# Kernel tuning notes

Hardware: AMD Instinct MI355X
Metric: run time of the kernel (lower is better)

## Reference

```python
import jax, jax.numpy as jnp
import numpy as np

N_NODES = 100_000
N_EDGES = 1_600_000
F_NODE = 16
F_EDGE = 8
HID = 128
N_GRAPHS = 2048


def setup_inputs() -> dict:
    key = jax.random.key(0)
    ks = jax.random.split(key, 20)
    inp = {
        "node_attr": jax.random.normal(ks[0], (N_NODES, F_NODE), dtype=jnp.float32),
        "edge_attr": jax.random.normal(ks[1], (N_EDGES, F_EDGE), dtype=jnp.float32),
        "edge_index": jax.random.randint(ks[2], (2, N_EDGES), 0, N_NODES),
        "adj_index": jax.random.randint(ks[3], (2, N_EDGES), 0, N_NODES),
        "adj_value": jax.random.uniform(ks[4], (N_EDGES,), dtype=jnp.float32) * 0.1,
        "batch": jnp.sort(jax.random.randint(ks[5], (N_NODES,), 0, N_GRAPHS)),
    }
    def glorot(k, shape):
        fan_in, fan_out = shape[0], shape[1]
        std = jnp.sqrt(2.0 / (fan_in + fan_out)).astype(jnp.float32)
        return jax.random.normal(k, shape, dtype=jnp.float32) * std
    # attr embedder params
    inp["W_node"] = glorot(ks[6], (F_NODE, HID))
    inp["W_edge"] = glorot(ks[7], (F_EDGE, HID))
    inp["b_embed"] = jnp.zeros((HID,), dtype=jnp.float32)
    # 3 GCN layers
    inp["W1"] = glorot(ks[8], (HID, HID)); inp["b1"] = jnp.zeros((HID,), jnp.float32)
    inp["W2"] = glorot(ks[9], (HID, HID)); inp["b2"] = jnp.zeros((HID,), jnp.float32)
    inp["W3"] = glorot(ks[10], (HID, HID)); inp["b3"] = jnp.zeros((HID,), jnp.float32)
    # predictor MLP
    inp["Wp1"] = glorot(ks[11], (HID, HID)); inp["bp1"] = jnp.full((HID,), 0.01, jnp.float32)
    inp["Wp2"] = glorot(ks[12], (HID, 1));   inp["bp2"] = jnp.full((1,), 0.01, jnp.float32)
    return inp


def _forward(node_attr, edge_attr, adj_value,
             W_node, W_edge, b_embed, W1, b1, W2, b2, W3, b3,
             Wp1, bp1, Wp2, bp2, edge_index, adj_index, batch):
    # --- attr embedder: mix node feats with edge feats scattered to dst nodes ---
    he = edge_attr @ W_edge                                   # [E, H]
    agg = jax.ops.segment_sum(he, edge_index[1], num_segments=N_NODES)
    h = jax.nn.relu(node_attr @ W_node + agg + b_embed)       # [N, H]

    # --- GCN stack: h <- relu(tilde_A @ (h W) + b) via sparse COO SpMM ---
    src, dst = adj_index[0], adj_index[1]
    def gcn(h, W, b):
        hw = h @ W + b                                        # [N, H]
        msg = adj_value[:, None] * hw[dst]                    # [E, H] gather
        return jax.nn.relu(jax.ops.segment_sum(msg, src, num_segments=N_NODES))
    h = gcn(h, W1, b1)
    h = gcn(h, W2, b2)
    h = gcn(h, W3, b3)

    # --- global_add_pool over graphs ---
    fp = jax.ops.segment_sum(h, batch, num_segments=N_GRAPHS)  # [G, H]

    # --- predictor MLP ---
    z = jax.nn.relu(fp @ Wp1 + bp1)
    return z @ Wp2 + bp2                                       # [G, 1]


def reference(node_attr, edge_attr, edge_index, adj_index, adj_value, batch,
              W_node, W_edge, b_embed, W1, b1, W2, b2, W3, b3,
              Wp1, bp1, Wp2, bp2):
    return _forward(node_attr, edge_attr, adj_value,
                    W_node, W_edge, b_embed, W1, b1, W2, b2, W3, b3,
                    Wp1, bp1, Wp2, bp2, edge_index, adj_index, batch)
```

## Files before the change

### kernel.cpp

```cpp
#include <hip/hip_runtime.h>

#define H 128
#define FN 16
#define FE 8
#define NBUK_MAX 1600

__global__ __launch_bounds__(256) void k_hist2_gb(
    const int* __restrict__ k1, const int* __restrict__ k2,
    int* __restrict__ bcnt1, int* __restrict__ bcnt2, int E, int nbuk,
    const int* __restrict__ batch, int* __restrict__ gstart, int N, int G) {
  if (blockIdx.x >= 512) {
    int n = (blockIdx.x - 512) * 256 + threadIdx.x;
    if (n > N) return;
    if (n == 0) {
      for (int g = 0; g <= batch[0]; g++) gstart[g] = 0;
    } else if (n == N) {
      for (int g = batch[N - 1] + 1; g <= G; g++) gstart[g] = N;
    } else {
      int b0 = batch[n - 1], b1 = batch[n];
      for (int g = b0 + 1; g <= b1; g++) gstart[g] = n;
    }
    return;
  }
  __shared__ int h1[NBUK_MAX], h2[NBUK_MAX];
  for (int i = threadIdx.x; i < nbuk; i += 256) { h1[i] = 0; h2[i] = 0; }
  __syncthreads();
  for (int e = blockIdx.x * 256 + threadIdx.x; e < E; e += 512 * 256) {
    atomicAdd(&h1[k1[e] >> 6], 1);
    atomicAdd(&h2[k2[e] >> 6], 1);
  }
  __syncthreads();
  for (int i = threadIdx.x; i < nbuk; i += 256) {
    if (h1[i]) atomicAdd(&bcnt1[i], h1[i]);
    if (h2[i]) atomicAdd(&bcnt2[i], h2[i]);
  }
}

__global__ __launch_bounds__(1024) void k_scan(
    const int* __restrict__ cnt1, int* __restrict__ st1, int* __restrict__ gc1,
    const int* __restrict__ cnt2, int* __restrict__ st2, int* __restrict__ gc2,
    int nbuk) {
  __shared__ int s[1024];
  int tid = threadIdx.x;
  for (int pass = 0; pass < 2; pass++) {
    const int* cnt = pass ? cnt2 : cnt1;
    int* st = pass ? st2 : st1;
    int* gc = pass ? gc2 : gc1;
    int run = 0;
    for (int half = 0; half * 1024 < nbuk; half++) {
      int i = half * 1024 + tid;
      int v = (i < nbuk) ? cnt[i] : 0;
      s[tid] = v; __syncthreads();
      for (int off = 1; off < 1024; off <<= 1) {
        int t = (tid >= off) ? s[tid - off] : 0;
        __syncthreads();
        s[tid] += t;
        __syncthreads();
      }
      int excl = run + s[tid] - v;
      if (i < nbuk) { st[i] = excl; gc[i] = excl; }
      run += s[1023];
      __syncthreads();
    }
    if (tid == 0) st[nbuk] = run;
    __syncthreads();
  }
}

__global__ __launch_bounds__(256) void k_p1_both(
    const int* __restrict__ k1, const int* __restrict__ adj, const float* __restrict__ vals,
    int* __restrict__ gcur1, int* __restrict__ gcur2,
    int* __restrict__ pkey, int2* __restrict__ bpay, int E, int nbuk, int p1b) {
  __shared__ int hc[NBUK_MAX];
  int tid = threadIdx.x;
  bool packed = (int)blockIdx.x < p1b;
  int chunk = packed ? blockIdx.x : blockIdx.x - p1b;
  const int* key = packed ? k1 : adj;
  int* gcur = packed ? gcur1 : gcur2;
  int c0 = chunk * 8192;
  int c1 = min(c0 + 8192, E);
  for (int i = tid; i < nbuk; i += 256) hc[i] = 0;
  __syncthreads();
  for (int e = c0 + tid; e < c1; e += 256)
    atomicAdd(&hc[key[e] >> 6], 1);
  __syncthreads();
  for (int i = tid; i < nbuk; i += 256) {
    int c = hc[i];
    if (c) hc[i] = atomicAdd(&gcur[i], c);
  }
  __syncthreads();
  if (packed) {
    for (int e = c0 + tid; e < c1; e += 256) {
      int k = key[e];
      int pos = atomicAdd(&hc[k >> 6], 1);
      pkey[pos] = (e << 6) | (k & 63);
    }
  } else {
    const int* dsts = adj + E;
    for (int e = c0 + tid; e < c1; e += 256) {
      int k = key[e];
      int pos = atomicAdd(&hc[k >> 6], 1);
      bpay[pos] = make_int2(dsts[e] | ((k & 63) << 20), __float_as_int(vals[e]));
    }
  }
}

__global__ __launch_bounds__(256) void k_agg_p2(
    const int* __restrict__ pkey, const float* __restrict__ edge_attr,
    const int* __restrict__ bst1,
    const float* __restrict__ node_attr, const float* __restrict__ Wn,
    const float* __restrict__ We8, const float* __restrict__ bemb,
    float* __restrict__ hout,
    const int2* __restrict__ bpay, const int* __restrict__ bst2,
    int* __restrict__ offs, int2* __restrict__ payF, float* __restrict__ rs,
    int N, int E, int nbuk) {
  __shared__ float lds[FE][64];
  __shared__ float na[64][FN];
  __shared__ int cnt[64], scn[64], cur[64];
  __shared__ float vsum[64];
  int tid = threadIdx.x;

  if ((int)blockIdx.x < nbuk) {
    int b = blockIdx.x;
    int node0 = b * 64;
    int col = tid & 127;
    int half = tid >> 7;
    float wreg[FN + FE];
#pragma unroll
    for (int k = 0; k < FN; k++) wreg[k] = Wn[k * H + col];
#pragma unroll
    for (int k = 0; k < FE; k++) wreg[FN + k] = We8[k * H + col];
    float bcol = bemb[col];

    for (int i = tid; i < FE * 64; i += 256) ((float*)lds)[i] = 0.f;
    for (int i = tid; i < 64 * FN; i += 256) {
      int n = node0 + (i >> 4);
      na[i >> 4][i & 15] = (n < N) ? node_attr[(size_t)n * FN + (i & 15)] : 0.f;
    }
    __syncthreads();
    int s = bst1[b], t = bst1[b + 1];
    int i = s + tid;
    for (; i + 256 < t; i += 512) {
      int pk0 = pkey[i], pk1 = pkey[i + 256];
      const float4* e0 = (const float4*)(edge_attr + (size_t)(pk0 >> 6) * FE);
      const float4* e1 = (const float4*)(edge_attr + (size_t)(pk1 >> 6) * FE);
      float4 a0 = e0[0], b0 = e0[1], a1 = e1[0], b1 = e1[1];
      int s0 = pk0 & 63, s1 = pk1 & 63;
      atomicAdd(&lds[0][s0], a0.x);  atomicAdd(&lds[1][s0], a0.y);
      atomicAdd(&lds[2][s0], a0.z);  atomicAdd(&lds[3][s0], a0.w);
      atomicAdd(&lds[4][s0], b0.x);  atomicAdd(&lds[5][s0], b0.y);
      atomicAdd(&lds[6][s0], b0.z);  atomicAdd(&lds[7][s0], b0.w);
      atomicAdd(&lds[0][s1], a1.x);  atomicAdd(&lds[1][s1], a1.y);
      atomicAdd(&lds[2][s1], a1.z);  atomicAdd(&lds[3][s1], a1.w);
      atomicAdd(&lds[4][s1], b1.x);  atomicAdd(&lds[5][s1], b1.y);
      atomicAdd(&lds[6][s1], b1.z);  atomicAdd(&lds[7][s1], b1.w);
    }
    for (; i < t; i += 256) {
      int pk = pkey[i];
      int e = pk >> 6, slot = pk & 63;
      const float4* ea = (const float4*)(edge_attr + (size_t)e * FE);
      float4 a = ea[0], b4 = ea[1];
      atomicAdd(&lds[0][slot], a.x);  atomicAdd(&lds[1][slot], a.y);
      atomicAdd(&lds[2][slot], a.z);  atomicAdd(&lds[3][slot], a.w);
      atomicAdd(&lds[4][slot], b4.x); atomicAdd(&lds[5][slot], b4.y);
      atomicAdd(&lds[6][slot], b4.z); atomicAdd(&lds[7][slot], b4.w);
    }
    __syncthreads();
    for (int pr = 0; pr < 32; pr++) {
      int nl = pr * 2 + half;
      int n = node0 + nl;
      float acc = bcol;
#pragma unroll
      for (int k = 0; k < FN; k++) acc += na[nl][k] * wreg[k];
#pragma unroll
      for (int k = 0; k < FE; k++) acc += lds[k][nl] * wreg[FN + k];
      if (n < N) hout[(size_t)n * H + col] = fmaxf(acc, 0.f);
    }
  } else {
    int b = blockIdx.x - nbuk;
    int s = bst2[b], t = bst2[b + 1];
    if (tid < 64) { cnt[tid] = 0; vsum[tid] = 0.f; }
    __syncthreads();
    for (int i = s + tid; i < t; i += 256) atomicAdd(&cnt[(bpay[i].x >> 20) & 63], 1);
    __syncthreads();
    if (tid < 64) scn[tid] = cnt[tid];
    __syncthreads();
    for (int off = 1; off < 64; off <<= 1) {
      int v = 0;
      if (tid < 64 && tid >= off) v = scn[tid - off];
      __syncthreads();
      if (tid < 64 && tid >= off) scn[tid] += v;
      __syncthreads();
    }
    if (tid < 64) {
      int excl = s + scn[tid] - cnt[tid];
      cur[tid] = excl;
      int node = b * 64 + tid;
      if (node < N) offs[node] = excl;
    }
    if (b == 0 && tid == 0) offs[N] = E;
    __syncthreads();
    for (int i = s + tid; i < t; i += 256) {
      int2 p = bpay[i];
      int slot = (p.x >> 20) & 63;
      int pos = atomicAdd(&cur[slot], 1);
      payF[pos] = make_int2(p.x & 0xFFFFF, p.y);
      atomicAdd(&vsum[slot], __int_as_float(p.y));
    }
    __syncthreads();
    if (tid < 64) {
      int node = b * 64 + tid;
      if (node < N) rs[node] = vsum[tid];
    }
  }
}

__global__ __launch_bounds__(256) void k_fused(
    const float* __restrict__ h, const int* __restrict__ offs,
    const int2* __restrict__ pay, const float* __restrict__ W,
    const float* __restrict__ bias, const float* __restrict__ rs,
    float* __restrict__ out, int N) {
  __shared__ float4 hs4[32 * 32];
  int tid = threadIdx.x;
  int c  = tid & 31;
  int rg = tid >> 5;
  int base = blockIdx.x * 32;
  const float4* h4 = (const float4*)h;

  for (int r = 0; r < 4; r++) {
    int row = rg * 4 + r;
    int n = base + row;
    float4 a0 = make_float4(0.f, 0.f, 0.f, 0.f);
    float4 a1 = make_float4(0.f, 0.f, 0.f, 0.f);
    float4 a2 = make_float4(0.f, 0.f, 0.f, 0.f);
    float4 a3 = make_float4(0.f, 0.f, 0.f, 0.f);
    if (n < N) {
      int s = offs[n], t = offs[n + 1];
      int i = s, t4 = s + ((t - s) & ~3);
      for (; i < t4; i += 4) {
        int2 p0 = pay[i], p1 = pay[i + 1], p2 = pay[i + 2], p3 = pay[i + 3];
        float4 h0 = h4[(size_t)p0.x * 32 + c];
        float4 h1 = h4[(size_t)p1.x * 32 + c];
        float4 h2 = h4[(size_t)p2.x * 32 + c];
        float4 h3 = h4[(size_t)p3.x * 32 + c];
        float v0 = __int_as_float(p0.y), v1 = __int_as_float(p1.y);
        float v2 = __int_as_float(p2.y), v3 = __int_as_float(p3.y);
        a0.x += v0 * h0.x; a0.y += v0 * h0.y; a0.z += v0 * h0.z; a0.w += v0 * h0.w;
        a1.x += v1 * h1.x; a1.y += v1 * h1.y; a1.z += v1 * h1.z; a1.w += v1 * h1.w;
        a2.x += v2 * h2.x; a2.y += v2 * h2.y; a2.z += v2 * h2.z; a2.w += v2 * h2.w;
        a3.x += v3 * h3.x; a3.y += v3 * h3.y; a3.z += v3 * h3.z; a3.w += v3 * h3.w;
      }
      for (; i < t; i++) {
        int2 p = pay[i];
        float v = __int_as_float(p.y);
        float4 hv = h4[(size_t)p.x * 32 + c];
        a0.x += v * hv.x; a0.y += v * hv.y; a0.z += v * hv.z; a0.w += v * hv.w;
      }
    }
    hs4[row * 32 + c] = make_float4(a0.x + a1.x + a2.x + a3.x,
                                    a0.y + a1.y + a2.y + a3.y,
                                    a0.z + a1.z + a2.z + a3.z,
                                    a0.w + a1.w + a2.w + a3.w);
  }
  __syncthreads();

  const float4* W4 = (const float4*)W;
  float4 acc[4];
#pragma unroll
  for (int i = 0; i < 4; i++) acc[i] = make_float4(0.f, 0.f, 0.f, 0.f);
#pragma unroll 2
  for (int k = 0; k < 32; k++) {
    float4 w0 = W4[(k * 4 + 0) * 32 + c];
    float4 w1 = W4[(k * 4 + 1) * 32 + c];
    float4 w2 = W4[(k * 4 + 2) * 32 + c];
    float4 w3 = W4[(k * 4 + 3) * 32 + c];
#pragma unroll
    for (int i = 0; i < 4; i++) {
      float4 hv = hs4[(rg + 8 * i) * 32 + k];
      acc[i].x += hv.x * w0.x + hv.y * w1.x + hv.z * w2.x + hv.w * w3.x;
      acc[i].y += hv.x * w0.y + hv.y * w1.y + hv.z * w2.y + hv.w * w3.y;
      acc[i].z += hv.x * w0.z + hv.y * w1.z + hv.z * w2.z + hv.w * w3.z;
      acc[i].w += hv.x * w0.w + hv.y * w1.w + hv.z * w2.w + hv.w * w3.w;
    }
  }

  float4 bv = ((const float4*)bias)[c];
#pragma unroll
  for (int i = 0; i < 4; i++) {
    int row = rg + 8 * i;
    int n = base + row;
    if (n < N) {
      float rsv = rs[n];
      float4 o;
      o.x = fmaxf(acc[i].x + rsv * bv.x, 0.f);
      o.y = fmaxf(acc[i].y + rsv * bv.y, 0.f);
      o.z = fmaxf(acc[i].z + rsv * bv.z, 0.f);
      o.w = fmaxf(acc[i].w + rsv * bv.w, 0.f);
      ((float4*)out)[(size_t)n * 32 + c] = o;
    }
  }
}

__global__ __launch_bounds__(256) void k_gemm_pred(
    const float* __restrict__ in, const float* __restrict__ W,
    const float* __restrict__ bias, const float* __restrict__ Wp2,
    const float* __restrict__ bp2, float* __restrict__ out, int N) {
  __shared__ float4 hs4[64 * 32];
  int tid = threadIdx.x;
  int c  = tid & 31;
  int rg = tid >> 5;
  int rowBase = blockIdx.x * 64;
  const float4* in4 = (const float4*)in;
  const float4* W4  = (const float4*)W;
#pragma unroll
  for (int j = 0; j < 8; j++) {
    int q = tid + 256 * j;
    int r = rowBase + (q >> 5);
    int rr = (r < N) ? r : (N - 1);
    hs4[q] = in4[(size_t)rr * 32 + (q & 31)];
  }
  __syncthreads();
  float4 acc[8];
#pragma unroll
  for (int i = 0; i < 8; i++) acc[i] = make_float4(0.f, 0.f, 0.f, 0.f);
#pragma unroll 2
  for (int k = 0; k < 32; k++) {
    float4 w0 = W4[(k * 4 + 0) * 32 + c];
    float4 w1 = W4[(k * 4 + 1) * 32 + c];
    float4 w2 = W4[(k * 4 + 2) * 32 + c];
    float4 w3 = W4[(k * 4 + 3) * 32 + c];
#pragma unroll
    for (int i = 0; i < 8; i++) {
      float4 hv = hs4[(rg + 8 * i) * 32 + k];
      acc[i].x += hv.x * w0.x + hv.y * w1.x + hv.z * w2.x + hv.w * w3.x;
      acc[i].y += hv.x * w0.y + hv.y * w1.y + hv.z * w2.y + hv.w * w3.y;
      acc[i].z += hv.x * w0.z + hv.y * w1.z + hv.z * w2.z + hv.w * w3.z;
      acc[i].w += hv.x * w0.w + hv.y * w1.w + hv.z * w2.w + hv.w * w3.w;
    }
  }
  float4 bv = ((const float4*)bias)[c];
  float4 wp = ((const float4*)Wp2)[c];
  float bp = bp2[0];
#pragma unroll
  for (int i = 0; i < 8; i++) {
    int row = rowBase + rg + 8 * i;
    float4 o;
    o.x = fmaxf(acc[i].x + bv.x, 0.f);
    o.y = fmaxf(acc[i].y + bv.y, 0.f);
    o.z = fmaxf(acc[i].z + bv.z, 0.f);
    o.w = fmaxf(acc[i].w + bv.w, 0.f);
    float v = o.x * wp.x + o.y * wp.y + o.z * wp.z + o.w * wp.w;
#pragma unroll
    for (int off = 16; off > 0; off >>= 1) v += __shfl_down(v, off, 32);
    if (c == 0 && row < N) out[row] = v + bp;
  }
}

__global__ __launch_bounds__(256) void k_pool_seg(
    const float* __restrict__ h, const int* __restrict__ gstart,
    float* __restrict__ fp, int G) {
  __shared__ float4 red[8][32];
  int g = blockIdx.x;
  int c = threadIdx.x & 31, rg = threadIdx.x >> 5;
  int s = gstart[g], t = gstart[g + 1];
  const float4* h4 = (const float4*)h;
  float4 a = make_float4(0.f, 0.f, 0.f, 0.f);
  for (int n = s + rg; n < t; n += 8) {
    float4 v = h4[(size_t)n * 32 + c];
    a.x += v.x; a.y += v.y; a.z += v.z; a.w += v.w;
  }
  red[rg][c] = a;
  __syncthreads();
  if (rg == 0) {
    float4 r = red[0][c];
#pragma unroll
    for (int j = 1; j < 8; j++) {
      float4 v = red[j][c];
      r.x += v.x; r.y += v.y; r.z += v.z; r.w += v.w;
    }
    ((float4*)fp)[(size_t)g * 32 + c] = r;
  }
}

extern "C" void kernel_launch(void* const* d_in, const int* in_sizes, int n_in,
                              void* d_out, int out_size, void* d_ws, size_t ws_size,
                              hipStream_t stream) {
  const float* node_attr  = (const float*)d_in[0];
  const float* edge_attr  = (const float*)d_in[1];
  const int*   edge_index = (const int*)d_in[2];
  const int*   adj_index  = (const int*)d_in[3];
  const float* adj_value  = (const float*)d_in[4];
  const int*   batch      = (const int*)d_in[5];
  const float* W_node  = (const float*)d_in[6];
  const float* W_edge  = (const float*)d_in[7];
  const float* b_embed = (const float*)d_in[8];
  const float* W1 = (const float*)d_in[9];
  const float* b1 = (const float*)d_in[10];
  const float* W2 = (const float*)d_in[11];
  const float* b2 = (const float*)d_in[12];
  const float* W3 = (const float*)d_in[13];
  const float* b3 = (const float*)d_in[14];
  const float* Wp1 = (const float*)d_in[15];
  const float* bp1 = (const float*)d_in[16];
  const float* Wp2 = (const float*)d_in[17];
  const float* bp2 = (const float*)d_in[18];
  float* out = (float*)d_out;

  const int E = in_sizes[4];
  const int N = in_sizes[5];
  const int G = out_size;
  const int nbuk = (N + 63) >> 6;
  const int p1b = (E + 8191) / 8192;
  const int gbB = (N + 256) / 256;

  float* A     = (float*)d_ws;
  float* B     = A + (size_t)N * H;
  int2*  payF  = (int2*)(B + (size_t)N * H);
  float* fpool = (float*)(payF + E);
  int*   bcnt1 = (int*)(fpool + (size_t)G * H);
  int*   bcnt2 = bcnt1 + nbuk;
  int*   bst1  = bcnt2 + nbuk;
  int*   gcur1 = bst1 + nbuk + 1;
  int*   bst2  = gcur1 + nbuk;
  int*   gcur2 = bst2 + nbuk + 1;
  int*   offs2 = gcur2 + nbuk;
  int*   gstart= offs2 + N + 1;
  float* rs    = (float*)(gstart + G + 1);
  int*   pkey  = (int*)B;
  int2*  bpay2 = (int2*)(((int*)B) + E);

  hipMemsetAsync(bcnt1, 0, (size_t)2 * nbuk * sizeof(int), stream);
  k_hist2_gb<<<512 + gbB, 256, 0, stream>>>(edge_index + E, adj_index, bcnt1, bcnt2,
                                            E, nbuk, batch, gstart, N, G);
  k_scan<<<1, 1024, 0, stream>>>(bcnt1, bst1, gcur1, bcnt2, bst2, gcur2, nbuk);

  k_p1_both<<<2 * p1b, 256, 0, stream>>>(edge_index + E, adj_index, adj_value,
                                         gcur1, gcur2, pkey, bpay2, E, nbuk, p1b);

  k_agg_p2<<<2 * nbuk, 256, 0, stream>>>(pkey, edge_attr, bst1,
                                         node_attr, W_node, W_edge, b_embed, A,
                                         bpay2, bst2, offs2, payF, rs, N, E, nbuk);

  int lb = (N + 31) / 32;
  k_fused<<<lb, 256, 0, stream>>>(A, offs2, payF, W1, b1, rs, B, N);
  k_fused<<<lb, 256, 0, stream>>>(B, offs2, payF, W2, b2, rs, A, N);
  k_fused<<<lb, 256, 0, stream>>>(A, offs2, payF, W3, b3, rs, B, N);

  k_pool_seg<<<G, 256, 0, stream>>>(B, gstart, fpool, G);
  k_gemm_pred<<<(G + 63) / 64, 256, 0, stream>>>(fpool, Wp1, bp1, Wp2, bp2, out, G);
}
```

Baseline: 900.7 us.

## Fuse global add pool into final GCN layer and enlarge node tile to 64

The last GCN layer now pools its outputs directly: each block reduces its 64 rows per graph in shared memory and atomically adds the result into the pooled buffer, so the final layer output never goes to global memory and the separate pool kernel and gstart computation are dropped. The fused SpMM+GEMM kernels also process 64 nodes per block instead of 32, which reuses each W load across more rows but doubles accumulator registers and shared memory per block. The pooled buffer is now zeroed by the existing memset, and float atomics make the pooled sums order-nondeterministic.

After: 856.3 us. 4.9% less time.

```diff
diff --git a/kernel.cpp b/kernel.cpp
--- a/kernel.cpp
+++ b/kernel.cpp
@@ -5,23 +5,9 @@
 #define FE 8
 #define NBUK_MAX 1600
 
-__global__ __launch_bounds__(256) void k_hist2_gb(
+__global__ __launch_bounds__(256) void k_hist2(
     const int* __restrict__ k1, const int* __restrict__ k2,
-    int* __restrict__ bcnt1, int* __restrict__ bcnt2, int E, int nbuk,
-    const int* __restrict__ batch, int* __restrict__ gstart, int N, int G) {
-  if (blockIdx.x >= 512) {
-    int n = (blockIdx.x - 512) * 256 + threadIdx.x;
-    if (n > N) return;
-    if (n == 0) {
-      for (int g = 0; g <= batch[0]; g++) gstart[g] = 0;
-    } else if (n == N) {
-      for (int g = batch[N - 1] + 1; g <= G; g++) gstart[g] = N;
-    } else {
-      int b0 = batch[n - 1], b1 = batch[n];
-      for (int g = b0 + 1; g <= b1; g++) gstart[g] = n;
-    }
-    return;
-  }
+    int* __restrict__ bcnt1, int* __restrict__ bcnt2, int E, int nbuk) {
   __shared__ int h1[NBUK_MAX], h2[NBUK_MAX];
   for (int i = threadIdx.x; i < nbuk; i += 256) { h1[i] = 0; h2[i] = 0; }
   __syncthreads();
@@ -220,15 +206,15 @@
     const int2* __restrict__ pay, const float* __restrict__ W,
     const float* __restrict__ bias, const float* __restrict__ rs,
     float* __restrict__ out, int N) {
-  __shared__ float4 hs4[32 * 32];
+  __shared__ float4 hs4[64 * 32];
   int tid = threadIdx.x;
   int c  = tid & 31;
   int rg = tid >> 5;
-  int base = blockIdx.x * 32;
+  int base = blockIdx.x * 64;
   const float4* h4 = (const float4*)h;
 
-  for (int r = 0; r < 4; r++) {
-    int row = rg * 4 + r;
+  for (int r = 0; r < 8; r++) {
+    int row = rg * 8 + r;
     int n = base + row;
     float4 a0 = make_float4(0.f, 0.f, 0.f, 0.f);
     float4 a1 = make_float4(0.f, 0.f, 0.f, 0.f);
@@ -265,9 +251,9 @@
   __syncthreads();
 
   const float4* W4 = (const float4*)W;
-  float4 acc[4];
-#pragma unroll
-  for (int i = 0; i < 4; i++) acc[i] = make_float4(0.f, 0.f, 0.f, 0.f);
+  float4 acc[8];
+#pragma unroll
+  for (int i = 0; i < 8; i++) acc[i] = make_float4(0.f, 0.f, 0.f, 0.f);
 #pragma unroll 2
   for (int k = 0; k < 32; k++) {
     float4 w0 = W4[(k * 4 + 0) * 32 + c];
@@ -275,7 +261,7 @@
     float4 w2 = W4[(k * 4 + 2) * 32 + c];
     float4 w3 = W4[(k * 4 + 3) * 32 + c];
 #pragma unroll
-    for (int i = 0; i < 4; i++) {
+    for (int i = 0; i < 8; i++) {
       float4 hv = hs4[(rg + 8 * i) * 32 + k];
       acc[i].x += hv.x * w0.x + hv.y * w1.x + hv.z * w2.x + hv.w * w3.x;
       acc[i].y += hv.x * w0.y + hv.y * w1.y + hv.z * w2.y + hv.w * w3.y;
@@ -286,7 +272,7 @@
 
   float4 bv = ((const float4*)bias)[c];
 #pragma unroll
-  for (int i = 0; i < 4; i++) {
+  for (int i = 0; i < 8; i++) {
     int row = rg + 8 * i;
     int n = base + row;
     if (n < N) {
@@ -298,6 +284,127 @@
       o.w = fmaxf(acc[i].w + rsv * bv.w, 0.f);
       ((float4*)out)[(size_t)n * 32 + c] = o;
     }
+  }
+}
+
+__global__ __launch_bounds__(256) void k_fused_pool(
+    const float* __restrict__ h, const int* __restrict__ offs,
+    const int2* __restrict__ pay, const float* __restrict__ W,
+    const float* __restrict__ bias, const float* __restrict__ rs,
+    const int* __restrict__ batch, float* __restrict__ fpool, int N) {
+  __shared__ float4 hs4[64 * 32];
+  __shared__ float4 psum[8][32];
+  __shared__ int btl[64];
+  int tid = threadIdx.x;
+  int c  = tid & 31;
+  int rg = tid >> 5;
+  int base = blockIdx.x * 64;
+  const float4* h4 = (const float4*)h;
+  if (tid < 64) btl[tid] = (base + tid < N) ? batch[base + tid] : -1;
+
+  for (int r = 0; r < 8; r++) {
+    int row = rg * 8 + r;
+    int n = base + row;
+    float4 a0 = make_float4(0.f, 0.f, 0.f, 0.f);
+    float4 a1 = make_float4(0.f, 0.f, 0.f, 0.f);
+    float4 a2 = make_float4(0.f, 0.f, 0.f, 0.f);
+    float4 a3 = make_float4(0.f, 0.f, 0.f, 0.f);
+    if (n < N) {
+      int s = offs[n], t = offs[n + 1];
+      int i = s, t4 = s + ((t - s) & ~3);
+      for (; i < t4; i += 4) {
+        int2 p0 = pay[i], p1 = pay[i + 1], p2 = pay[i + 2], p3 = pay[i + 3];
+        float4 h0 = h4[(size_t)p0.x * 32 + c];
+        float4 h1 = h4[(size_t)p1.x * 32 + c];
+        float4 h2 = h4[(size_t)p2.x * 32 + c];
+        float4 h3 = h4[(size_t)p3.x * 32 + c];
+        float v0 = __int_as_float(p0.y), v1 = __int_as_float(p1.y);
+        float v2 = __int_as_float(p2.y), v3 = __int_as_float(p3.y);
+        a0.x += v0 * h0.x; a0.y += v0 * h0.y; a0.z += v0 * h0.z; a0.w += v0 * h0.w;
+        a1.x += v1 * h1.x; a1.y += v1 * h1.y; a1.z += v1 * h1.z; a1.w += v1 * h1.w;
+        a2.x += v2 * h2.x; a2.y += v2 * h2.y; a2.z += v2 * h2.z; a2.w += v2 * h2.w;
+        a3.x += v3 * h3.x; a3.y += v3 * h3.y; a3.z += v3 * h3.z; a3.w += v3 * h3.w;
+      }
+      for (; i < t; i++) {
+        int2 p = pay[i];
+        float v = __int_as_float(p.y);
+        float4 hv = h4[(size_t)p.x * 32 + c];
+        a0.x += v * hv.x; a0.y += v * hv.y; a0.z += v * hv.z; a0.w += v * hv.w;
+      }
+    }
+    hs4[row * 32 + c] = make_float4(a0.x + a1.x + a2.x + a3.x,
+                                    a0.y + a1.y + a2.y + a3.y,
+                                    a0.z + a1.z + a2.z + a3.z,
+                                    a0.w + a1.w + a2.w + a3.w);
+  }
+  __syncthreads();
+
+  const float4* W4 = (const float4*)W;
+  float4 acc[8];
+#pragma unroll
+  for (int i = 0; i < 8; i++) acc[i] = make_float4(0.f, 0.f, 0.f, 0.f);
+#pragma unroll 2
+  for (int k = 0; k < 32; k++) {
+    float4 w0 = W4[(k * 4 + 0) * 32 + c];
+    float4 w1 = W4[(k * 4 + 1) * 32 + c];
+    float4 w2 = W4[(k * 4 + 2) * 32 + c];
+    float4 w3 = W4[(k * 4 + 3) * 32 + c];
+#pragma unroll
+    for (int i = 0; i < 8; i++) {
+      float4 hv = hs4[(rg + 8 * i) * 32 + k];
+      acc[i].x += hv.x * w0.x + hv.y * w1.x + hv.z * w2.x + hv.w * w3.x;
+      acc[i].y += hv.x * w0.y + hv.y * w1.y + hv.z * w2.y + hv.w * w3.y;
+      acc[i].z += hv.x * w0.z + hv.y * w1.z + hv.z * w2.z + hv.w * w3.z;
+      acc[i].w += hv.x * w0.w + hv.y * w1.w + hv.z * w2.w + hv.w * w3.w;
+    }
+  }
+
+  float4 bv = ((const float4*)bias)[c];
+  __syncthreads();
+#pragma unroll
+  for (int i = 0; i < 8; i++) {
+    int row = rg + 8 * i;
+    int n = base + row;
+    float4 o = make_float4(0.f, 0.f, 0.f, 0.f);
+    if (n < N) {
+      float rsv = rs[n];
+      o.x = fmaxf(acc[i].x + rsv * bv.x, 0.f);
+      o.y = fmaxf(acc[i].y + rsv * bv.y, 0.f);
+      o.z = fmaxf(acc[i].z + rsv * bv.z, 0.f);
+      o.w = fmaxf(acc[i].w + rsv * bv.w, 0.f);
+    }
+    hs4[row * 32 + c] = o;
+  }
+  __syncthreads();
+
+  int g0 = btl[0];
+  int g1 = g0;
+  for (int r = 1; r < 64; r++) { int bb = btl[r]; if (bb >= 0) g1 = bb; }
+  for (int gr = g0; gr <= g1; gr++) {
+    float4 s = make_float4(0.f, 0.f, 0.f, 0.f);
+#pragma unroll
+    for (int r = rg * 8; r < rg * 8 + 8; r++) {
+      if (btl[r] == gr) {
+        float4 v = hs4[r * 32 + c];
+        s.x += v.x; s.y += v.y; s.z += v.z; s.w += v.w;
+      }
+    }
+    psum[rg][c] = s;
+    __syncthreads();
+    if (rg == 0) {
+      float4 tot = psum[0][c];
+#pragma unroll
+      for (int j = 1; j < 8; j++) {
+        float4 v = psum[j][c];
+        tot.x += v.x; tot.y += v.y; tot.z += v.z; tot.w += v.w;
+      }
+      float* dst = fpool + (size_t)gr * H + c * 4;
+      atomicAdd(dst + 0, tot.x);
+      atomicAdd(dst + 1, tot.y);
+      atomicAdd(dst + 2, tot.z);
+      atomicAdd(dst + 3, tot.w);
+    }
+    __syncthreads();
   }
 }
 
@@ -353,32 +460,6 @@
 #pragma unroll
     for (int off = 16; off > 0; off >>= 1) v += __shfl_down(v, off, 32);
     if (c == 0 && row < N) out[row] = v + bp;
-  }
-}
-
-__global__ __launch_bounds__(256) void k_pool_seg(
-    const float* __restrict__ h, const int* __restrict__ gstart,
-    float* __restrict__ fp, int G) {
-  __shared__ float4 red[8][32];
-  int g = blockIdx.x;
-  int c = threadIdx.x & 31, rg = threadIdx.x >> 5;
-  int s = gstart[g], t = gstart[g + 1];
-  const float4* h4 = (const float4*)h;
-  float4 a = make_float4(0.f, 0.f, 0.f, 0.f);
-  for (int n = s + rg; n < t; n += 8) {
-    float4 v = h4[(size_t)n * 32 + c];
-    a.x += v.x; a.y += v.y; a.z += v.z; a.w += v.w;
-  }
-  red[rg][c] = a;
-  __syncthreads();
-  if (rg == 0) {
-    float4 r = red[0][c];
-#pragma unroll
-    for (int j = 1; j < 8; j++) {
-      float4 v = red[j][c];
-      r.x += v.x; r.y += v.y; r.z += v.z; r.w += v.w;
-    }
-    ((float4*)fp)[(size_t)g * 32 + c] = r;
   }
 }
 
@@ -411,7 +492,6 @@
   const int G = out_size;
   const int nbuk = (N + 63) >> 6;
   const int p1b = (E + 8191) / 8192;
-  const int gbB = (N + 256) / 256;
 
   float* A     = (float*)d_ws;
   float* B     = A + (size_t)N * H;
@@ -424,14 +504,12 @@
   int*   bst2  = gcur1 + nbuk;
   int*   gcur2 = bst2 + nbuk + 1;
   int*   offs2 = gcur2 + nbuk;
-  int*   gstart= offs2 + N + 1;
-  float* rs    = (float*)(gstart + G + 1);
+  float* rs    = (float*)(offs2 + N + 1);
   int*   pkey  = (int*)B;
   int2*  bpay2 = (int2*)(((int*)B) + E);
 
-  hipMemsetAsync(bcnt1, 0, (size_t)2 * nbuk * sizeof(int), stream);
-  k_hist2_gb<<<512 + gbB, 256, 0, stream>>>(edge_index + E, adj_index, bcnt1, bcnt2,
-                                            E, nbuk, batch, gstart, N, G);
+  hipMemsetAsync(fpool, 0, (size_t)G * H * sizeof(float) + 2 * nbuk * sizeof(int), stream);
+  k_hist2<<<512, 256, 0, stream>>>(edge_index + E, adj_index, bcnt1, bcnt2, E, nbuk);
   k_scan<<<1, 1024, 0, stream>>>(bcnt1, bst1, gcur1, bcnt2, bst2, gcur2, nbuk);
 
   k_p1_both<<<2 * p1b, 256, 0, stream>>>(edge_index + E, adj_index, adj_value,
@@ -441,11 +519,10 @@
                                          node_attr, W_node, W_edge, b_embed, A,
                                          bpay2, bst2, offs2, payF, rs, N, E, nbuk);
 
-  int lb = (N + 31) / 32;
+  int lb = (N + 63) / 64;
   k_fused<<<lb, 256, 0, stream>>>(A, offs2, payF, W1, b1, rs, B, N);
   k_fused<<<lb, 256, 0, stream>>>(B, offs2, payF, W2, b2, rs, A, N);
-  k_fused<<<lb, 256, 0, stream>>>(A, offs2, payF, W3, b3, rs, B, N);
-
-  k_pool_seg<<<G, 256, 0, stream>>>(B, gstart, fpool, G);
+  k_fused_pool<<<lb, 256, 0, stream>>>(A, offs2, payF, W3, b3, rs, batch, fpool, N);
+
   k_gemm_pred<<<(G + 63) / 64, 256, 0, stream>>>(fpool, Wp1, bp1, Wp2, bp2, out, G);
 }
```
